# Kernel tuning notes

Hardware: AMD Instinct MI355X
Metric: run time of the kernel (lower is better)

Reference implementation:

```python
import jax, jax.numpy as jnp
import numpy as np


def setup_inputs() -> dict:
    key = jax.random.key(0)
    kq, kv = jax.random.split(key)
    N, To, Ti, H = 8, 1024, 4096, 512
    queries = jax.random.normal(kq, (N, To, H), dtype=jnp.float32)
    values = jax.random.normal(kv, (N, Ti, H), dtype=jnp.float32)
    return {"queries": queries, "values": values}


def reference(queries, values):
    # scores: N x To x Ti (unscaled, unmasked dot-product attention)
    scores = jnp.einsum("noh,nih->noi", queries, values)
    attn = jax.nn.softmax(scores, axis=-1)          # softmax over Ti
    out = jnp.einsum("noi,nih->noh", attn, values)  # N x To x H
    return out, attn
```

## Files before the change

kernel.cpp:

```cpp
#include <hip/hip_runtime.h>
#include <hip/hip_bf16.h>

typedef __bf16 bf16x8 __attribute__((ext_vector_type(8)));
typedef __bf16 bf16x4 __attribute__((ext_vector_type(4)));
typedef float  f32x4  __attribute__((ext_vector_type(4)));

constexpr int N_  = 8;
constexpr int TO_ = 1024;
constexpr int TI_ = 4096;
constexpr int H_  = 512;

__device__ inline void split8(const float4& x0, const float4& x1,
                              bf16x8& h, bf16x8& l)
{
    float xs[8] = {x0.x, x0.y, x0.z, x0.w, x1.x, x1.y, x1.z, x1.w};
#pragma unroll
    for (int i = 0; i < 8; ++i) {
        __bf16 hh = (__bf16)xs[i];
        h[i] = hh;
        l[i] = (__bf16)(xs[i] - (float)hh);
    }
}

__global__ __launch_bounds__(256)
void split_kernel(const float* __restrict__ X, __bf16* __restrict__ Xh,
                  __bf16* __restrict__ Xl)
{
    const size_t idx = ((size_t)blockIdx.x * 256 + threadIdx.x) * 8;
    const float4* src = reinterpret_cast<const float4*>(X + idx);
    float4 x0 = src[0], x1 = src[1];
    bf16x8 h, l;
    split8(x0, x1, h, l);
    *reinterpret_cast<bf16x8*>(Xh + idx) = h;
    *reinterpret_cast<bf16x8*>(Xl + idx) = l;
}

__global__ __launch_bounds__(256)
void vt2_kernel(const __bf16* __restrict__ Vh, __bf16* __restrict__ Vt)
{
    const int hb = blockIdx.x, tb = blockIdx.y, n = blockIdx.z;
    const int h  = hb * 64 + (threadIdx.x >> 2);
    const int tq = threadIdx.x & 3;
    const __bf16* Vn = Vh + (size_t)n * TI_ * H_;
    __bf16* Vtn = Vt + (size_t)n * H_ * TI_;

#pragma unroll
    for (int j = 0; j < 16; ++j) {
        const int t0 = tb * 512 + tq * 128 + j * 8;
        bf16x8 o;
#pragma unroll
        for (int e = 0; e < 8; ++e)
            o[e] = Vn[(size_t)(t0 + e) * H_ + h];
        *reinterpret_cast<bf16x8*>(&Vtn[(size_t)h * TI_ + t0]) = o;
    }
}

__global__ __launch_bounds__(512, 2)
void qk4_kernel(const __bf16* __restrict__ Qh, const __bf16* __restrict__ Ql,
                const __bf16* __restrict__ Vh, const __bf16* __restrict__ Vl,
                float* __restrict__ S)
{
    __shared__ __bf16 AhA[128 * 64], AhB[128 * 64];
    __shared__ __bf16 AlA[128 * 64], AlB[128 * 64];
    __shared__ __bf16 BhA[128 * 64], BhB[128 * 64];
    __shared__ __bf16 BlA[128 * 64], BlB[128 * 64];

    const int tt = blockIdx.x, mt = blockIdx.y, n = blockIdx.z;
    const size_t qoff = ((size_t)n * TO_ + (size_t)mt * 128) * H_;
    const size_t voff = ((size_t)n * TI_ + (size_t)tt * 128) * H_;
    const __bf16* Qhb = Qh + qoff;
    const __bf16* Qlb = Ql + qoff;
    const __bf16* Vhb = Vh + voff;
    const __bf16* Vlb = Vl + voff;

    const int tid  = threadIdx.x;
    const int lane = tid & 63, wave = tid >> 6;
    const int wm = wave >> 1, wc = wave & 1;
    const int fr = lane & 15, fq = lane >> 4;

    auto stage1 = [&](const __bf16* __restrict__ g, __bf16* lds, int k0) {
#pragma unroll
        for (int i = 0; i < 2; ++i) {
            const int q   = i * 512 + tid;
            const int row = q >> 3, c = q & 7;
            const int csw = c ^ (row & 7);
            const __bf16* gs = g + (size_t)row * H_ + k0 + csw * 8;
            const int q0 = (i * 512 + wave * 64) * 16;
            __builtin_amdgcn_global_load_lds(
                (const __attribute__((address_space(1))) void*)gs,
                (__attribute__((address_space(3))) void*)((char*)lds + q0),
                16, 0, 0);
        }
    };
    auto stage = [&](__bf16* ah, __bf16* al, __bf16* bh, __bf16* bl, int k0) {
        stage1(Qhb, ah, k0);
        stage1(Qlb, al, k0);
        stage1(Vhb, bh, k0);
        stage1(Vlb, bl, k0);
    };

    f32x4 acc[2][4] = {};

    auto compute = [&](const __bf16* Ah, const __bf16* Al,
                       const __bf16* Bh, const __bf16* Bl) {
#pragma unroll
        for (int kk = 0; kk < 2; ++kk) {
            bf16x8 ah[2], al[2], bh[4], bl[4];
#pragma unroll
            for (int m = 0; m < 2; ++m) {
                const int row = wm * 32 + m * 16 + fr;
                const int cs  = (kk * 4 + fq) ^ (row & 7);
                ah[m] = *reinterpret_cast<const bf16x8*>(&Ah[row * 64 + cs * 8]);
                al[m] = *reinterpret_cast<const bf16x8*>(&Al[row * 64 + cs * 8]);
            }
#pragma unroll
            for (int j = 0; j < 4; ++j) {
                const int row = wc * 64 + j * 16 + fr;
                const int cs  = (kk * 4 + fq) ^ (row & 7);
                bh[j] = *reinterpret_cast<const bf16x8*>(&Bh[row * 64 + cs * 8]);
                bl[j] = *reinterpret_cast<const bf16x8*>(&Bl[row * 64 + cs * 8]);
            }
#pragma unroll
            for (int m = 0; m < 2; ++m)
#pragma unroll
                for (int j = 0; j < 4; ++j) {
                    acc[m][j] = __builtin_amdgcn_mfma_f32_16x16x32_bf16(ah[m], bh[j], acc[m][j], 0, 0, 0);
                    acc[m][j] = __builtin_amdgcn_mfma_f32_16x16x32_bf16(ah[m], bl[j], acc[m][j], 0, 0, 0);
                    acc[m][j] = __builtin_amdgcn_mfma_f32_16x16x32_bf16(al[m], bh[j], acc[m][j], 0, 0, 0);
                }
        }
    };

    constexpr int NT = H_ / 64;
    stage(AhA, AlA, BhA, BlA, 0);
    __syncthreads();
    for (int kt = 0; kt < NT; kt += 2) {
        if (kt + 1 < NT) stage(AhB, AlB, BhB, BlB, (kt + 1) * 64);
        compute(AhA, AlA, BhA, BlA);
        __syncthreads();
        if (kt + 2 < NT) stage(AhA, AlA, BhA, BlA, (kt + 2) * 64);
        compute(AhB, AlB, BhB, BlB);
        __syncthreads();
    }

    float* Sb = S + ((size_t)n * TO_ + (size_t)mt * 128) * TI_ + (size_t)tt * 128;
    const int crow0 = wm * 32 + fq * 4;
    const int ccol0 = wc * 64 + fr;
#pragma unroll
    for (int m = 0; m < 2; ++m)
#pragma unroll
        for (int j = 0; j < 4; ++j)
#pragma unroll
            for (int r = 0; r < 4; ++r)
                Sb[(size_t)(crow0 + m * 16 + r) * TI_ + (ccol0 + j * 16)] = acc[m][j][r];
}

__global__ __launch_bounds__(256)
void softmax2_kernel(float* __restrict__ S, __bf16* __restrict__ A16)
{
    const int wave = threadIdx.x >> 6, lane = threadIdx.x & 63;
    const size_t row = (size_t)blockIdx.x * 4 + wave;
    float4* p = reinterpret_cast<float4*>(S + row * TI_);
    __bf16* p16 = A16 + row * TI_;

    float4 v[16];
    float m = -3.0e38f;
#pragma unroll
    for (int j = 0; j < 16; ++j) {
        v[j] = p[j * 64 + lane];
        m = fmaxf(m, fmaxf(fmaxf(v[j].x, v[j].y), fmaxf(v[j].z, v[j].w)));
    }
#pragma unroll
    for (int s = 32; s > 0; s >>= 1) m = fmaxf(m, __shfl_xor(m, s));

    constexpr float L2E = 1.4426950408889634f;
    float sum = 0.f;
#pragma unroll
    for (int j = 0; j < 16; ++j) {
        v[j].x = exp2f((v[j].x - m) * L2E);
        v[j].y = exp2f((v[j].y - m) * L2E);
        v[j].z = exp2f((v[j].z - m) * L2E);
        v[j].w = exp2f((v[j].w - m) * L2E);
        sum += (v[j].x + v[j].y) + (v[j].z + v[j].w);
    }
#pragma unroll
    for (int s = 32; s > 0; s >>= 1) sum += __shfl_xor(sum, s);

    const float inv = 1.0f / sum;
#pragma unroll
    for (int j = 0; j < 16; ++j) {
        v[j].x *= inv; v[j].y *= inv; v[j].z *= inv; v[j].w *= inv;
        p[j * 64 + lane] = v[j];
        bf16x4 o;
        o[0] = (__bf16)v[j].x; o[1] = (__bf16)v[j].y;
        o[2] = (__bf16)v[j].z; o[3] = (__bf16)v[j].w;
        *reinterpret_cast<bf16x4*>(&p16[(j * 64 + lane) * 4]) = o;
    }
}

__global__ __launch_bounds__(512, 2)
void pv7_kernel(const __bf16* __restrict__ A16, const __bf16* __restrict__ Vt,
                float* __restrict__ O, float* __restrict__ P)
{
    __shared__ __bf16 AsmA[128 * 64], AsmB[128 * 64];
    __shared__ __bf16 BsmA[256 * 64], BsmB[256 * 64];

    const int flat = blockIdx.x;
    const int mt = flat >> 5;
    const int g  = flat & 31;
    const int n  = g >> 2;
    const int ht = (g >> 1) & 1;
    const int kc = g & 1;

    const __bf16* Ab = A16 + ((size_t)n * TO_ + (size_t)mt * 128) * TI_ + (size_t)kc * 2048;
    const __bf16* Bb = Vt  + ((size_t)n * H_  + (size_t)ht * 256) * TI_ + (size_t)kc * 2048;

    const int tid = threadIdx.x, lane = tid & 63, wave = tid >> 6;
    const int wm = wave >> 2, wh = wave & 3;
    const int fr = lane & 15, fq = lane >> 4;

    auto stage = [&](__bf16* asm_, __bf16* bsm_, int k0) {
#pragma unroll
        for (int i = 0; i < 2; ++i) {
            const int q   = i * 512 + tid;
            const int row = q >> 3, c = q & 7;
            const int csw = c ^ (row & 7);
            const __bf16* gs = Ab + (size_t)row * TI_ + k0 + csw * 8;
            const int q0 = (i * 512 + wave * 64) * 16;
            __builtin_amdgcn_global_load_lds(
                (const __attribute__((address_space(1))) void*)gs,
                (__attribute__((address_space(3))) void*)((char*)asm_ + q0),
                16, 0, 0);
        }
#pragma unroll
        for (int i = 0; i < 4; ++i) {
            const int q   = i * 512 + tid;
            const int row = q >> 3, c = q & 7;
            const int csw = c ^ (row & 7);
            const __bf16* gs = Bb + (size_t)row * TI_ + k0 + csw * 8;
            const int q0 = (i * 512 + wave * 64) * 16;
            __builtin_amdgcn_global_load_lds(
                (const __attribute__((address_space(1))) void*)gs,
                (__attribute__((address_space(3))) void*)((char*)bsm_ + q0),
                16, 0, 0);
        }
    };

    f32x4 acc[4][4] = {};

    auto compute = [&](const __bf16* Asm, const __bf16* Bsm) {
#pragma unroll
        for (int kk = 0; kk < 2; ++kk) {
            bf16x8 a[4], b[4];
#pragma unroll
            for (int m = 0; m < 4; ++m) {
                const int row = wm * 64 + m * 16 + fr;
                const int cs  = (kk * 4 + fq) ^ (row & 7);
                a[m] = *reinterpret_cast<const bf16x8*>(&Asm[row * 64 + cs * 8]);
            }
#pragma unroll
            for (int j = 0; j < 4; ++j) {
                const int row = wh * 64 + j * 16 + fr;
                const int cs  = (kk * 4 + fq) ^ (row & 7);
                b[j] = *reinterpret_cast<const bf16x8*>(&Bsm[row * 64 + cs * 8]);
            }
#pragma unroll
            for (int m = 0; m < 4; ++m)
#pragma unroll
                for (int j = 0; j < 4; ++j)
                    acc[m][j] = __builtin_amdgcn_mfma_f32_16x16x32_bf16(
                        a[m], b[j], acc[m][j], 0, 0, 0);
        }
    };

    constexpr int NT = 2048 / 64;
    stage(AsmA, BsmA, 0);
    __syncthreads();
    for (int kt = 0; kt < NT; kt += 2) {
        if (kt + 1 < NT) stage(AsmB, BsmB, (kt + 1) * 64);
        compute(AsmA, BsmA);
        __syncthreads();
        if (kt + 2 < NT) stage(AsmA, BsmA, (kt + 2) * 64);
        compute(AsmB, BsmB);
        __syncthreads();
    }

    float* D  = (kc == 0) ? O : P;
    float* Db = D + ((size_t)n * TO_ + (size_t)mt * 128) * H_ + ht * 256;
#pragma unroll
    for (int m = 0; m < 4; ++m) {
        const int orow = wm * 64 + m * 16 + fq * 4;
#pragma unroll
        for (int j = 0; j < 4; ++j) {
            const int ocol = wh * 64 + j * 16 + fr;
#pragma unroll
            for (int r = 0; r < 4; ++r)
                Db[(size_t)(orow + r) * H_ + ocol] = acc[m][j][r];
        }
    }
}

__global__ __launch_bounds__(256)
void add_kernel(float4* __restrict__ o, const float4* __restrict__ p)
{
    const size_t i = (size_t)blockIdx.x * 256 + threadIdx.x;
    float4 a = o[i], b = p[i];
    a.x += b.x; a.y += b.y; a.z += b.z; a.w += b.w;
    o[i] = a;
}

constexpr int BM1 = 128, BN1 = 128, BK1 = 32, LP1 = BK1 + 8;

__global__ __launch_bounds__(256, 2)
void qk_kernel(const float* __restrict__ Q, const float* __restrict__ V,
               float* __restrict__ S)
{
    __shared__ __bf16 Ah[BM1 * LP1];
    __shared__ __bf16 Al[BM1 * LP1];
    __shared__ __bf16 Bh[BN1 * LP1];
    __shared__ __bf16 Bl[BN1 * LP1];

    const int tt = blockIdx.x, mt = blockIdx.y, n = blockIdx.z;
    const float* Qb = Q + ((size_t)n * TO_ + (size_t)mt * BM1) * H_;
    const float* Vb = V + ((size_t)n * TI_ + (size_t)tt * BN1) * H_;

    const int tid  = threadIdx.x;
    const int lane = tid & 63, wave = tid >> 6;
    const int wr = wave >> 1, wc = wave & 1;
    const int srow = tid >> 2, scg = tid & 3;

    f32x4 acc[4][4] = {};

    for (int k0 = 0; k0 < H_; k0 += BK1) {
        __syncthreads();
#pragma unroll
        for (int half = 0; half < 2; ++half) {
            const int r = srow + half * 64;
            {
                const float4* src =
                    reinterpret_cast<const float4*>(Qb + (size_t)r * H_ + k0 + scg * 8);
                float4 x0 = src[0], x1 = src[1];
                bf16x8 hv, lv;
                split8(x0, x1, hv, lv);
                *reinterpret_cast<bf16x8*>(&Ah[r * LP1 + scg * 8]) = hv;
                *reinterpret_cast<bf16x8*>(&Al[r * LP1 + scg * 8]) = lv;
            }
            {
                const float4* src =
                    reinterpret_cast<const float4*>(Vb + (size_t)r * H_ + k0 + scg * 8);
                float4 x0 = src[0], x1 = src[1];
                bf16x8 hv, lv;
                split8(x0, x1, hv, lv);
                *reinterpret_cast<bf16x8*>(&Bh[r * LP1 + scg * 8]) = hv;
                *reinterpret_cast<bf16x8*>(&Bl[r * LP1 + scg * 8]) = lv;
            }
        }
        __syncthreads();

        bf16x8 ah[4], al[4], bh[4], bl[4];
        const int fr = lane & 15, fg = (lane >> 4) * 8;
#pragma unroll
        for (int m = 0; m < 4; ++m) {
            const int row = wr * 64 + m * 16 + fr;
            ah[m] = *reinterpret_cast<const bf16x8*>(&Ah[row * LP1 + fg]);
            al[m] = *reinterpret_cast<const bf16x8*>(&Al[row * LP1 + fg]);
        }
#pragma unroll
        for (int j = 0; j < 4; ++j) {
            const int row = wc * 64 + j * 16 + fr;
            bh[j] = *reinterpret_cast<const bf16x8*>(&Bh[row * LP1 + fg]);
            bl[j] = *reinterpret_cast<const bf16x8*>(&Bl[row * LP1 + fg]);
        }
#pragma unroll
        for (int m = 0; m < 4; ++m)
#pragma unroll
            for (int j = 0; j < 4; ++j) {
                acc[m][j] = __builtin_amdgcn_mfma_f32_16x16x32_bf16(ah[m], bh[j], acc[m][j], 0, 0, 0);
                acc[m][j] = __builtin_amdgcn_mfma_f32_16x16x32_bf16(ah[m], bl[j], acc[m][j], 0, 0, 0);
                acc[m][j] = __builtin_amdgcn_mfma_f32_16x16x32_bf16(al[m], bh[j], acc[m][j], 0, 0, 0);
            }
    }

    float* Sb = S + ((size_t)n * TO_ + (size_t)mt * BM1) * TI_ + (size_t)tt * BN1;
    const int crow0 = wr * 64 + (lane >> 4) * 4;
    const int ccol0 = wc * 64 + (lane & 15);
#pragma unroll
    for (int m = 0; m < 4; ++m)
#pragma unroll
        for (int j = 0; j < 4; ++j)
#pragma unroll
            for (int r = 0; r < 4; ++r)
                Sb[(size_t)(crow0 + m * 16 + r) * TI_ + (ccol0 + j * 16)] = acc[m][j][r];
}

__global__ __launch_bounds__(256)
void softmax_kernel(float* __restrict__ S)
{
    const int wave = threadIdx.x >> 6, lane = threadIdx.x & 63;
    const size_t row = (size_t)blockIdx.x * 4 + wave;
    float4* p = reinterpret_cast<float4*>(S + row * TI_);

    float4 v[16];
    float m = -3.0e38f;
#pragma unroll
    for (int j = 0; j < 16; ++j) {
        v[j] = p[j * 64 + lane];
        m = fmaxf(m, fmaxf(fmaxf(v[j].x, v[j].y), fmaxf(v[j].z, v[j].w)));
    }
#pragma unroll
    for (int s = 32; s > 0; s >>= 1) m = fmaxf(m, __shfl_xor(m, s));

    constexpr float L2E = 1.4426950408889634f;
    float sum = 0.f;
#pragma unroll
    for (int j = 0; j < 16; ++j) {
        v[j].x = exp2f((v[j].x - m) * L2E);
        v[j].y = exp2f((v[j].y - m) * L2E);
        v[j].z = exp2f((v[j].z - m) * L2E);
        v[j].w = exp2f((v[j].w - m) * L2E);
        sum += (v[j].x + v[j].y) + (v[j].z + v[j].w);
    }
#pragma unroll
    for (int s = 32; s > 0; s >>= 1) sum += __shfl_xor(sum, s);

    const float inv = 1.0f / sum;
#pragma unroll
    for (int j = 0; j < 16; ++j) {
        v[j].x *= inv; v[j].y *= inv; v[j].z *= inv; v[j].w *= inv;
        p[j * 64 + lane] = v[j];
    }
}

__global__ __launch_bounds__(256)
void vt_kernel(const float* __restrict__ V, __bf16* __restrict__ Vt)
{
    const int hb = blockIdx.x, tb = blockIdx.y, n = blockIdx.z;
    const int h  = hb * 64 + (threadIdx.x >> 2);
    const int tq = threadIdx.x & 3;
    const float* Vn = V + (size_t)n * TI_ * H_;
    __bf16* Vtn = Vt + (size_t)n * H_ * TI_;

#pragma unroll
    for (int j = 0; j < 16; ++j) {
        const int t0 = tb * 512 + tq * 128 + j * 8;
        bf16x8 o;
#pragma unroll
        for (int e = 0; e < 8; ++e)
            o[e] = (__bf16)Vn[(size_t)(t0 + e) * H_ + h];
        *reinterpret_cast<bf16x8*>(&Vtn[(size_t)h * TI_ + t0]) = o;
    }
}

constexpr int PBM = 32, PBK = 64, PLP = PBK + 8;

__global__ __launch_bounds__(512, 2)
void pv_fast_kernel(const float* __restrict__ A, const __bf16* __restrict__ Vt,
                    float* __restrict__ O)
{
    __shared__ __bf16 AsmF[PBM * PLP];
    __shared__ __bf16 BsmF[512 * PLP];

    const int n = blockIdx.x, mt = blockIdx.y;
    const float*  Ab = A  + ((size_t)n * TO_ + (size_t)mt * PBM) * TI_;
    const __bf16* Vb = Vt + (size_t)n * H_ * TI_;

    const int tid = threadIdx.x, lane = tid & 63, wv = tid >> 6;
    const int ar = tid >> 4;
    const int ac = (tid & 15) * 4;
    const int bh = tid >> 3;
    const int bc = (tid & 7) * 8;

    float4 aReg;
    bf16x8 bReg[8];

    auto loadTile = [&](int k0) {
        aReg = *reinterpret_cast<const float4*>(Ab + (size_t)ar * TI_ + k0 + ac);
#pragma unroll
        for (int i = 0; i < 8; ++i)
            bReg[i] = *reinterpret_cast<const bf16x8*>(
                Vb + (size_t)(bh + i * 64) * TI_ + k0 + bc);
    };

    f32x4 acc[2][4] = {};
    const int fr = lane & 15, fg = (lane >> 4) * 8;

    loadTile(0);
    constexpr int NT = TI_ / PBK;
    for (int kt = 0; kt < NT; ++kt) {
        __syncthreads();
        {
            bf16x4 av;
            av[0] = (__bf16)aReg.x; av[1] = (__bf16)aReg.y;
            av[2] = (__bf16)aReg.z; av[3] = (__bf16)aReg.w;
            *reinterpret_cast<bf16x4*>(&AsmF[ar * PLP + ac]) = av;
#pragma unroll
            for (int i = 0; i < 8; ++i)
                *reinterpret_cast<bf16x8*>(&BsmF[(bh + i * 64) * PLP + bc]) = bReg[i];
        }
        __syncthreads();
        if (kt + 1 < NT) loadTile((kt + 1) * PBK);

#pragma unroll
        for (int kk = 0; kk < 2; ++kk) {
            bf16x8 af[2], bfr[4];
#pragma unroll
            for (int m = 0; m < 2; ++m)
                af[m] = *reinterpret_cast<const bf16x8*>(
                    &AsmF[(m * 16 + fr) * PLP + kk * 32 + fg]);
#pragma unroll
            for (int j = 0; j < 4; ++j)
                bfr[j] = *reinterpret_cast<const bf16x8*>(
                    &BsmF[(wv * 64 + j * 16 + fr) * PLP + kk * 32 + fg]);
#pragma unroll
            for (int m = 0; m < 2; ++m)
#pragma unroll
                for (int j = 0; j < 4; ++j)
                    acc[m][j] = __builtin_amdgcn_mfma_f32_16x16x32_bf16(
                        af[m], bfr[j], acc[m][j], 0, 0, 0);
        }
    }

    float* Ob = O + ((size_t)n * TO_ + (size_t)mt * PBM) * H_ + wv * 64;
    const int crow = (lane >> 4) * 4;
    const int ccol = lane & 15;
#pragma unroll
    for (int m = 0; m < 2; ++m)
#pragma unroll
        for (int j = 0; j < 4; ++j)
#pragma unroll
            for (int r = 0; r < 4; ++r)
                Ob[(size_t)(m * 16 + crow + r) * H_ + j * 16 + ccol] = acc[m][j][r];
}

extern "C" void kernel_launch(void* const* d_in, const int* in_sizes, int n_in,
                              void* d_out, int out_size, void* d_ws, size_t ws_size,
                              hipStream_t stream)
{
    const float* Q = (const float*)d_in[0];
    const float* V = (const float*)d_in[1];
    float* out  = (float*)d_out;
    float* attn = out + (size_t)N_ * TO_ * H_;

    const size_t NV = (size_t)N_ * TI_ * H_;
    const size_t NQ = (size_t)N_ * TO_ * H_;
    const size_t FULL_BYTES = (3 * NV + 2 * NQ) * sizeof(__bf16);
    const size_t VT_BYTES   = NV * sizeof(__bf16);

    __bf16* wsb = (__bf16*)d_ws;
    __bf16* Vt = wsb;
    __bf16* Vh = wsb + NV;
    __bf16* Vl = wsb + 2 * NV;
    __bf16* Qh = wsb + 3 * NV;
    __bf16* Ql = wsb + 3 * NV + NQ;
    __bf16* A16 = wsb + NV;
    float*  Ppart = (float*)(wsb + 3 * NV);

    if (ws_size >= FULL_BYTES) {
        split_kernel<<<dim3(NV / (256 * 8)), 256, 0, stream>>>(V, Vh, Vl);
        split_kernel<<<dim3(NQ / (256 * 8)), 256, 0, stream>>>(Q, Qh, Ql);
        vt2_kernel<<<dim3(H_ / 64, TI_ / 512, N_), 256, 0, stream>>>(Vh, Vt);
        qk4_kernel<<<dim3(TI_ / 128, TO_ / 128, N_), 512, 0, stream>>>(Qh, Ql, Vh, Vl, attn);
        softmax2_kernel<<<dim3(N_ * TO_ / 4), 256, 0, stream>>>(attn, A16);
        pv7_kernel<<<dim3(256), 512, 0, stream>>>(A16, Vt, out, Ppart);
        add_kernel<<<dim3((unsigned)(NQ / 4 / 256)), 256, 0, stream>>>(
            (float4*)out, (const float4*)Ppart);
    } else if (ws_size >= VT_BYTES) {
        vt_kernel<<<dim3(H_ / 64, TI_ / 512, N_), 256, 0, stream>>>(V, Vt);
        qk_kernel<<<dim3(TI_ / BN1, TO_ / BM1, N_), 256, 0, stream>>>(Q, V, attn);
        softmax_kernel<<<dim3(N_ * TO_ / 4), 256, 0, stream>>>(attn);
        pv_fast_kernel<<<dim3(N_, TO_ / PBM), 512, 0, stream>>>(attn, Vt, out);
    }
}
```

Baseline: 262.6 us.

## Replace double-buffered 512-thread QK kernel with single-buffer 256-thread variant

The QK score kernel moves from 8 waves with double-buffered LDS to 4 waves, each computing a 64x64 tile, with a single LDS buffer and two barriers per k-step. This halves LDS use per block (64KB to 32KB) and doubles per-wave register accumulators, so occupancy and reuse per wave change. In exchange it loses the overlap of global-to-LDS loads with MFMA compute that the ping-pong buffering provided.

```diff
diff --git a/kernel.cpp b/kernel.cpp
--- a/kernel.cpp
+++ b/kernel.cpp
@@ -55,15 +55,15 @@
     }
 }
 
-__global__ __launch_bounds__(512, 2)
-void qk4_kernel(const __bf16* __restrict__ Qh, const __bf16* __restrict__ Ql,
+__global__ __launch_bounds__(256, 2)
+void qk3_kernel(const __bf16* __restrict__ Qh, const __bf16* __restrict__ Ql,
                 const __bf16* __restrict__ Vh, const __bf16* __restrict__ Vl,
                 float* __restrict__ S)
 {
-    __shared__ __bf16 AhA[128 * 64], AhB[128 * 64];
-    __shared__ __bf16 AlA[128 * 64], AlB[128 * 64];
-    __shared__ __bf16 BhA[128 * 64], BhB[128 * 64];
-    __shared__ __bf16 BlA[128 * 64], BlB[128 * 64];
+    __shared__ __bf16 Ah[128 * 64];
+    __shared__ __bf16 Al[128 * 64];
+    __shared__ __bf16 Bh[128 * 64];
+    __shared__ __bf16 Bl[128 * 64];
 
     const int tt = blockIdx.x, mt = blockIdx.y, n = blockIdx.z;
     const size_t qoff = ((size_t)n * TO_ + (size_t)mt * 128) * H_;
@@ -75,40 +75,43 @@
 
     const int tid  = threadIdx.x;
     const int lane = tid & 63, wave = tid >> 6;
-    const int wm = wave >> 1, wc = wave & 1;
+    const int wr = wave >> 1, wc = wave & 1;
     const int fr = lane & 15, fq = lane >> 4;
 
-    auto stage1 = [&](const __bf16* __restrict__ g, __bf16* lds, int k0) {
-#pragma unroll
-        for (int i = 0; i < 2; ++i) {
-            const int q   = i * 512 + tid;
-            const int row = q >> 3, c = q & 7;
-            const int csw = c ^ (row & 7);
+    const int srow = tid >> 3;
+    const int sc   = tid & 7;
+
+    auto stage = [&](const __bf16* __restrict__ g, __bf16* lds, int k0) {
+#pragma unroll
+        for (int i = 0; i < 4; ++i) {
+            const int row = i * 32 + srow;
+            const int csw = sc ^ (row & 7);
             const __bf16* gs = g + (size_t)row * H_ + k0 + csw * 8;
-            const int q0 = (i * 512 + wave * 64) * 16;
+            const int q0 = (i * 256 + wave * 64) * 16;
             __builtin_amdgcn_global_load_lds(
                 (const __attribute__((address_space(1))) void*)gs,
                 (__attribute__((address_space(3))) void*)((char*)lds + q0),
                 16, 0, 0);
         }
     };
-    auto stage = [&](__bf16* ah, __bf16* al, __bf16* bh, __bf16* bl, int k0) {
-        stage1(Qhb, ah, k0);
-        stage1(Qlb, al, k0);
-        stage1(Vhb, bh, k0);
-        stage1(Vlb, bl, k0);
-    };
-
-    f32x4 acc[2][4] = {};
-
-    auto compute = [&](const __bf16* Ah, const __bf16* Al,
-                       const __bf16* Bh, const __bf16* Bl) {
+
+    f32x4 acc[4][4] = {};
+
+    for (int kt = 0; kt < H_ / 64; ++kt) {
+        const int k0 = kt * 64;
+        __syncthreads();
+        stage(Qhb, Ah, k0);
+        stage(Qlb, Al, k0);
+        stage(Vhb, Bh, k0);
+        stage(Vlb, Bl, k0);
+        __syncthreads();
+
 #pragma unroll
         for (int kk = 0; kk < 2; ++kk) {
-            bf16x8 ah[2], al[2], bh[4], bl[4];
-#pragma unroll
-            for (int m = 0; m < 2; ++m) {
-                const int row = wm * 32 + m * 16 + fr;
+            bf16x8 ah[4], al[4], bh[4], bl[4];
+#pragma unroll
+            for (int m = 0; m < 4; ++m) {
+                const int row = wr * 64 + m * 16 + fr;
                 const int cs  = (kk * 4 + fq) ^ (row & 7);
                 ah[m] = *reinterpret_cast<const bf16x8*>(&Ah[row * 64 + cs * 8]);
                 al[m] = *reinterpret_cast<const bf16x8*>(&Al[row * 64 + cs * 8]);
@@ -121,7 +124,7 @@
                 bl[j] = *reinterpret_cast<const bf16x8*>(&Bl[row * 64 + cs * 8]);
             }
 #pragma unroll
-            for (int m = 0; m < 2; ++m)
+            for (int m = 0; m < 4; ++m)
 #pragma unroll
                 for (int j = 0; j < 4; ++j) {
                     acc[m][j] = __builtin_amdgcn_mfma_f32_16x16x32_bf16(ah[m], bh[j], acc[m][j], 0, 0, 0);
@@ -129,25 +132,13 @@
                     acc[m][j] = __builtin_amdgcn_mfma_f32_16x16x32_bf16(al[m], bh[j], acc[m][j], 0, 0, 0);
                 }
         }
-    };
-
-    constexpr int NT = H_ / 64;
-    stage(AhA, AlA, BhA, BlA, 0);
-    __syncthreads();
-    for (int kt = 0; kt < NT; kt += 2) {
-        if (kt + 1 < NT) stage(AhB, AlB, BhB, BlB, (kt + 1) * 64);
-        compute(AhA, AlA, BhA, BlA);
-        __syncthreads();
-        if (kt + 2 < NT) stage(AhA, AlA, BhA, BlA, (kt + 2) * 64);
-        compute(AhB, AlB, BhB, BlB);
-        __syncthreads();
     }
 
     float* Sb = S + ((size_t)n * TO_ + (size_t)mt * 128) * TI_ + (size_t)tt * 128;
-    const int crow0 = wm * 32 + fq * 4;
+    const int crow0 = wr * 64 + fq * 4;
     const int ccol0 = wc * 64 + fr;
 #pragma unroll
-    for (int m = 0; m < 2; ++m)
+    for (int m = 0; m < 4; ++m)
 #pragma unroll
         for (int j = 0; j < 4; ++j)
 #pragma unroll
@@ -559,7 +550,7 @@
         split_kernel<<<dim3(NV / (256 * 8)), 256, 0, stream>>>(V, Vh, Vl);
         split_kernel<<<dim3(NQ / (256 * 8)), 256, 0, stream>>>(Q, Qh, Ql);
         vt2_kernel<<<dim3(H_ / 64, TI_ / 512, N_), 256, 0, stream>>>(Vh, Vt);
-        qk4_kernel<<<dim3(TI_ / 128, TO_ / 128, N_), 512, 0, stream>>>(Qh, Ql, Vh, Vl, attn);
+        qk3_kernel<<<dim3(TI_ / 128, TO_ / 128, N_), 256, 0, stream>>>(Qh, Ql, Vh, Vl, attn);
         softmax2_kernel<<<dim3(N_ * TO_ / 4), 256, 0, stream>>>(attn, A16);
         pv7_kernel<<<dim3(256), 512, 0, stream>>>(A16, Vt, out, Ppart);
         add_kernel<<<dim3((unsigned)(NQ / 4 / 256)), 256, 0, stream>>>(
```

Measured after the change: 250.5 us. 1.05x faster.

## Fuse V split with transpose and hand-schedule QK double-buffer waits

Applied to the files above, without the earlier changes.

V is now split into hi/lo bf16 and transposed in one kernel through an LDS tile, so the separate transpose pass that re-read Vh from global memory is gone. The QK kernel stages two K-tiles up front and replaces __syncthreads with raw barriers plus explicit vmcnt/lgkmcnt waits, so global loads for the next tile can stay in flight while the current one is computed. Launch bounds drop to one block per CU, which gives more registers but less occupancy. The hand-written waitcnt values assume a fixed count of outstanding loads per stage, which is fragile.

```diff
diff --git a/kernel.cpp b/kernel.cpp
--- a/kernel.cpp
+++ b/kernel.cpp
@@ -9,6 +9,11 @@
 constexpr int TO_ = 1024;
 constexpr int TI_ = 4096;
 constexpr int H_  = 512;
+
+#define SBAR()      __builtin_amdgcn_s_barrier()
+#define WAIT_VM8()  asm volatile("s_waitcnt vmcnt(8)" ::: "memory")
+#define WAIT_VM0()  asm volatile("s_waitcnt vmcnt(0)" ::: "memory")
+#define WAIT_LGKM() asm volatile("s_waitcnt lgkmcnt(0)" ::: "memory")
 
 __device__ inline void split8(const float4& x0, const float4& x1,
                               bf16x8& h, bf16x8& l)
@@ -36,27 +41,54 @@
 }
 
 __global__ __launch_bounds__(256)
-void vt2_kernel(const __bf16* __restrict__ Vh, __bf16* __restrict__ Vt)
-{
-    const int hb = blockIdx.x, tb = blockIdx.y, n = blockIdx.z;
-    const int h  = hb * 64 + (threadIdx.x >> 2);
+void splitv2_kernel(const float* __restrict__ V, __bf16* __restrict__ Vh,
+                    __bf16* __restrict__ Vl, __bf16* __restrict__ Vt)
+{
+    __shared__ __bf16 Lh[64][72];
+
+    const int tt = blockIdx.x, hb = blockIdx.y, n = blockIdx.z;
+    const int t0 = tt * 64, h0 = hb * 64;
+    const float* Vn = V + (size_t)n * TI_ * H_;
+    __bf16* Vhn = Vh + (size_t)n * TI_ * H_;
+    __bf16* Vln = Vl + (size_t)n * TI_ * H_;
+    __bf16* Vtn = Vt + (size_t)n * H_ * TI_;
+
+    const int tr = threadIdx.x >> 4;
+    const int hc = (threadIdx.x & 15) * 4;
+
+#pragma unroll
+    for (int j = 0; j < 4; ++j) {
+        const int t = tr + j * 16;
+        const size_t o = (size_t)(t0 + t) * H_ + h0 + hc;
+        float4 x = *reinterpret_cast<const float4*>(Vn + o);
+        bf16x4 hv, lv;
+        float xs[4] = {x.x, x.y, x.z, x.w};
+#pragma unroll
+        for (int e = 0; e < 4; ++e) {
+            __bf16 hh = (__bf16)xs[e];
+            hv[e] = hh;
+            lv[e] = (__bf16)(xs[e] - (float)hh);
+        }
+        *reinterpret_cast<bf16x4*>(Vhn + o) = hv;
+        *reinterpret_cast<bf16x4*>(Vln + o) = lv;
+        *reinterpret_cast<bf16x4*>(&Lh[t][hc]) = hv;
+    }
+    __syncthreads();
+
+    const int th = threadIdx.x >> 2;
     const int tq = threadIdx.x & 3;
-    const __bf16* Vn = Vh + (size_t)n * TI_ * H_;
-    __bf16* Vtn = Vt + (size_t)n * H_ * TI_;
-
-#pragma unroll
-    for (int j = 0; j < 16; ++j) {
-        const int t0 = tb * 512 + tq * 128 + j * 8;
+#pragma unroll
+    for (int s = 0; s < 2; ++s) {
+        const int tb = tq * 16 + s * 8;
         bf16x8 o;
 #pragma unroll
-        for (int e = 0; e < 8; ++e)
-            o[e] = Vn[(size_t)(t0 + e) * H_ + h];
-        *reinterpret_cast<bf16x8*>(&Vtn[(size_t)h * TI_ + t0]) = o;
-    }
-}
-
-__global__ __launch_bounds__(512, 2)
-void qk4_kernel(const __bf16* __restrict__ Qh, const __bf16* __restrict__ Ql,
+        for (int e = 0; e < 8; ++e) o[e] = Lh[tb + e][th];
+        *reinterpret_cast<bf16x8*>(&Vtn[(size_t)(h0 + th) * TI_ + t0 + tb]) = o;
+    }
+}
+
+__global__ __launch_bounds__(512, 1)
+void qk7_kernel(const __bf16* __restrict__ Qh, const __bf16* __restrict__ Ql,
                 const __bf16* __restrict__ Vh, const __bf16* __restrict__ Vl,
                 float* __restrict__ S)
 {
@@ -133,14 +165,35 @@
 
     constexpr int NT = H_ / 64;
     stage(AhA, AlA, BhA, BlA, 0);
-    __syncthreads();
+    stage(AhB, AlB, BhB, BlB, 64);
+    WAIT_VM8();
+    SBAR();
+
+#pragma unroll
     for (int kt = 0; kt < NT; kt += 2) {
-        if (kt + 1 < NT) stage(AhB, AlB, BhB, BlB, (kt + 1) * 64);
         compute(AhA, AlA, BhA, BlA);
-        __syncthreads();
-        if (kt + 2 < NT) stage(AhA, AlA, BhA, BlA, (kt + 2) * 64);
+        WAIT_LGKM();
+        SBAR();
+        if (kt + 2 < NT) {
+            stage(AhA, AlA, BhA, BlA, (kt + 2) * 64);
+            WAIT_VM8();
+        } else {
+            WAIT_VM0();
+        }
+        SBAR();
+
         compute(AhB, AlB, BhB, BlB);
-        __syncthreads();
+        if (kt + 2 < NT) {
+            WAIT_LGKM();
+            SBAR();
+            if (kt + 3 < NT) {
+                stage(AhB, AlB, BhB, BlB, (kt + 3) * 64);
+                WAIT_VM8();
+            } else {
+                WAIT_VM0();
+            }
+            SBAR();
+        }
     }
 
     float* Sb = S + ((size_t)n * TO_ + (size_t)mt * 128) * TI_ + (size_t)tt * 128;
@@ -556,10 +609,9 @@
     float*  Ppart = (float*)(wsb + 3 * NV);
 
     if (ws_size >= FULL_BYTES) {
-        split_kernel<<<dim3(NV / (256 * 8)), 256, 0, stream>>>(V, Vh, Vl);
+        splitv2_kernel<<<dim3(TI_ / 64, H_ / 64, N_), 256, 0, stream>>>(V, Vh, Vl, Vt);
         split_kernel<<<dim3(NQ / (256 * 8)), 256, 0, stream>>>(Q, Qh, Ql);
-        vt2_kernel<<<dim3(H_ / 64, TI_ / 512, N_), 256, 0, stream>>>(Vh, Vt);
-        qk4_kernel<<<dim3(TI_ / 128, TO_ / 128, N_), 512, 0, stream>>>(Qh, Ql, Vh, Vl, attn);
+        qk7_kernel<<<dim3(TI_ / 128, TO_ / 128, N_), 512, 0, stream>>>(Qh, Ql, Vh, Vl, attn);
         softmax2_kernel<<<dim3(N_ * TO_ / 4), 256, 0, stream>>>(attn, A16);
         pv7_kernel<<<dim3(256), 512, 0, stream>>>(A16, Vt, out, Ppart);
         add_kernel<<<dim3((unsigned)(NQ / 4 / 256)), 256, 0, stream>>>(
```

New measurement: 257.2 us. -2.0%, faster.
